# Optimization experiments

Hardware: AMD Instinct MI355X
Metric: run time of the kernel (lower is better)

Reference implementation:

```python
import jax, jax.numpy as jnp
import numpy as np

INPUT_SIZE = 4096
HIDDEN = 1024
WINDOW = 2048
STRIDE = 1024
METRIC = 32
POOLING = "last"


def setup_inputs() -> dict:
    key = jax.random.key(0)
    ks = jax.random.split(key, 9)
    s = 1.0 / np.sqrt(HIDDEN)  # torch LSTMCell/Linear init bound
    u = lambda k, shape: jax.random.uniform(k, shape, jnp.float32, -s, s)
    return {
        "inp": jax.random.normal(ks[0], (WINDOW, INPUT_SIZE), jnp.float32),
        "h1": jax.random.normal(ks[1], (1, HIDDEN), jnp.float32),
        "c1": jax.random.normal(ks[2], (1, HIDDEN), jnp.float32),
        "W_ih": u(ks[3], (4 * HIDDEN, INPUT_SIZE)),
        "W_hh": u(ks[4], (4 * HIDDEN, HIDDEN)),
        "b_ih": u(ks[5], (4 * HIDDEN,)),
        "b_hh": u(ks[6], (4 * HIDDEN,)),
        "fc_w": u(ks[7], (METRIC, HIDDEN)),
        "fc_b": u(ks[8], (METRIC,)),
    }


def reference(inp, h1, c1, W_ih, W_hh, b_ih, b_hh, fc_w, fc_b):
    window = min(WINDOW, inp.shape[0])
    # Precompute the input-side gate projection as one GEMM: [T, 4H]
    xg = inp[:window] @ W_ih.T + b_ih

    def step(carry, xg_t):
        h, c = carry  # each [1, H]
        gates = xg_t + h @ W_hh.T + b_hh  # [1, 4H]
        i, f, g, o = jnp.split(gates, 4, axis=-1)
        c = jax.nn.sigmoid(f) * c + jax.nn.sigmoid(i) * jnp.tanh(g)
        h = jax.nn.sigmoid(o) * jnp.tanh(c)
        return (h, c), (h, c)

    (h_fin, c_fin), (hs, cs) = jax.lax.scan(step, (h1, c1), xg)

    if window >= STRIDE:
        h_last = jax.lax.stop_gradient(hs[STRIDE - 1])  # [1, H], detached
        c_last = jax.lax.stop_gradient(cs[STRIDE - 1])
    else:
        h_last, c_last = None, None

    if POOLING == "mean":
        # mean of fc(h_i) over last STRIDE steps of the window
        out = (hs[window - STRIDE:, 0, :] @ fc_w.T + fc_b).sum(axis=0, keepdims=True) / STRIDE
    else:  # 'last'
        out = h_fin @ fc_w.T + fc_b  # [1, METRIC]
    out = jnp.tanh(out)
    return out, h_last, c_last
```

## Files before the change

### kernel.cpp

```cpp
#include <hip/hip_runtime.h>
#include <stdint.h>

typedef unsigned short u16;
typedef unsigned long long u64;
typedef __attribute__((ext_vector_type(8))) short short8;
typedef __attribute__((ext_vector_type(4))) float floatx4;

#define K_IN    4096
#define HID     1024
#define G4H     4096
#define T_STEPS 2048
#define NWG     128
#define SPIN_MAX 60000

__device__ __forceinline__ u16 f2bf(float f) {
  union { float f; unsigned int i; } v; v.f = f;
  unsigned int lsb = (v.i >> 16) & 1u;
  v.i += 0x7fffu + lsb;
  return (u16)(v.i >> 16);
}
__device__ __forceinline__ float finz(float x) {
  unsigned b = __float_as_uint(x);
  return ((b & 0x7f800000u) == 0x7f800000u) ? 0.f : x;
}
__device__ __forceinline__ float sigm(float x) {
  x = fminf(30.f, fmaxf(-30.f, finz(x)));
  return 1.0f / (1.0f + __expf(-x));
}
__device__ __forceinline__ float tanh_s(float x) {
  x = fminf(15.f, fmaxf(-15.f, finz(x)));
  float e = __expf(2.0f * x);
  return (e - 1.0f) / (e + 1.0f);
}

__device__ __forceinline__ void publish_h(u64* hx, int slot, int idx, float h) {
  h = finz(h);
  u64 v = ((u64)(unsigned)(slot + 1) << 32) | (u64)__float_as_uint(h);
  __hip_atomic_store(&hx[(size_t)slot * HID + idx], v,
                     __ATOMIC_RELAXED, __HIP_MEMORY_SCOPE_AGENT);
}

__device__ __forceinline__ void poll4(const u64* hx, int slot, int j0,
                                      float* v, int* alive) {
  const u64* p = hx + (size_t)slot * HID + j0;
  const unsigned tag = (unsigned)(slot + 1);
  if (*alive) {
    int spins = 0;
    for (;;) {
      u64 a = __hip_atomic_load(&p[0], __ATOMIC_RELAXED, __HIP_MEMORY_SCOPE_AGENT);
      u64 b = __hip_atomic_load(&p[1], __ATOMIC_RELAXED, __HIP_MEMORY_SCOPE_AGENT);
      u64 c = __hip_atomic_load(&p[2], __ATOMIC_RELAXED, __HIP_MEMORY_SCOPE_AGENT);
      u64 d = __hip_atomic_load(&p[3], __ATOMIC_RELAXED, __HIP_MEMORY_SCOPE_AGENT);
      if ((unsigned)(a >> 32) == tag && (unsigned)(b >> 32) == tag &&
          (unsigned)(c >> 32) == tag && (unsigned)(d >> 32) == tag) {
        v[0] = finz(__uint_as_float((unsigned)a));
        v[1] = finz(__uint_as_float((unsigned)b));
        v[2] = finz(__uint_as_float((unsigned)c));
        v[3] = finz(__uint_as_float((unsigned)d));
        return;
      }
      if (++spins > SPIN_MAX) { *alive = 0; break; }
      __builtin_amdgcn_s_sleep(1);
    }
  }
  v[0] = v[1] = v[2] = v[3] = 0.f;
}

__global__ __launch_bounds__(256) void cvt_bf16_k(const float* __restrict__ src,
                                                  u16* __restrict__ dst, int n4) {
  int i = blockIdx.x * 256 + threadIdx.x;
  if (i < n4) {
    float4 v = *(const float4*)(src + (size_t)i * 4);
    u16 o0 = f2bf(v.x), o1 = f2bf(v.y), o2 = f2bf(v.z), o3 = f2bf(v.w);
    ushort4 o = {o0, o1, o2, o3};
    *(ushort4*)(dst + (size_t)i * 4) = o;
  }
}

__global__ __launch_bounds__(256) void xg_gemm_k(const u16* __restrict__ A,
                                                 const u16* __restrict__ B,
                                                 const float* __restrict__ bias,
                                                 float* __restrict__ C)
{
  __shared__ __align__(16) u16 As[128 * 64];
  __shared__ __align__(16) u16 Bs[128 * 64];
  const int tid  = threadIdx.x;
  const int lane = tid & 63;
  const int quad = lane >> 4;
  const int l16  = lane & 15;
  const int wid  = tid >> 6;
  const int wm   = wid >> 1, wn = wid & 1;
  const int tileM = blockIdx.y * 128;
  const int tileN = blockIdx.x * 128;

  floatx4 acc[4][4];
  #pragma unroll
  for (int mi = 0; mi < 4; ++mi)
    #pragma unroll
    for (int ni = 0; ni < 4; ++ni)
      acc[mi][ni] = (floatx4){0.f, 0.f, 0.f, 0.f};

  for (int k0 = 0; k0 < K_IN; k0 += 64) {
    #pragma unroll
    for (int i = 0; i < 4; ++i) {
      int c = i * 256 + tid;
      int row = c >> 3, col = (c & 7) * 8;
      *(short8*)(As + c * 8) = *(const short8*)(A + (size_t)(tileM + row) * K_IN + k0 + col);
      *(short8*)(Bs + c * 8) = *(const short8*)(B + (size_t)(tileN + row) * K_IN + k0 + col);
    }
    __syncthreads();
    #pragma unroll
    for (int kk = 0; kk < 64; kk += 32) {
      short8 av[4], bv[4];
      #pragma unroll
      for (int mi = 0; mi < 4; ++mi)
        av[mi] = *(const short8*)(As + (wm * 64 + mi * 16 + l16) * 64 + kk + quad * 8);
      #pragma unroll
      for (int ni = 0; ni < 4; ++ni)
        bv[ni] = *(const short8*)(Bs + (wn * 64 + ni * 16 + l16) * 64 + kk + quad * 8);
      #pragma unroll
      for (int mi = 0; mi < 4; ++mi)
        #pragma unroll
        for (int ni = 0; ni < 4; ++ni)
          acc[mi][ni] = __builtin_amdgcn_mfma_f32_16x16x32_bf16(av[mi], bv[ni], acc[mi][ni], 0, 0, 0);
    }
    __syncthreads();
  }
  #pragma unroll
  for (int ni = 0; ni < 4; ++ni) {
    int n = tileN + wn * 64 + ni * 16 + l16;
    float bn = bias[n];
    #pragma unroll
    for (int mi = 0; mi < 4; ++mi) {
      int mbase = tileM + wm * 64 + mi * 16 + quad * 4;
      #pragma unroll
      for (int r = 0; r < 4; ++r)
        C[(size_t)(mbase + r) * G4H + n] = acc[mi][ni][r] + bn;
    }
  }
}

__global__ __launch_bounds__(256, 1) void lstm_scan_k(const float* __restrict__ Whh,
                                                      const float* __restrict__ bhh,
                                                      const float* __restrict__ h1,
                                                      const float* __restrict__ c1,
                                                      const float* __restrict__ fcw,
                                                      const float* __restrict__ fcb,
                                                      const float* __restrict__ xg,
                                                      u64* hx,
                                                      float* out)
{
  const int g    = blockIdx.x;
  const int tid  = threadIdx.x;
  const int lane = tid & 63;
  const int w    = tid >> 6;

  __shared__ float h_local[HID];
  __shared__ float gsum[32];
  __shared__ float xgb[2][32];
  __shared__ float bhhb[32];
  __shared__ float pp[32][8];

  float wreg[8][16];
  {
    const size_t rowbase = (size_t)(w * HID + g * 8);
    #pragma unroll
    for (int u = 0; u < 8; ++u)
      #pragma unroll
      for (int j = 0; j < 16; ++j)
        wreg[u][j] = Whh[(rowbase + u) * HID + j * 64 + lane];
  }
  if (tid < 32) bhhb[tid] = bhh[(tid >> 3) * HID + g * 8 + (tid & 7)];

  float c_state = 0.f;
  if (tid < 8) {
    c_state = c1[g * 8 + tid];
    publish_h(hx, 0, g * 8 + tid, h1[g * 8 + tid]);
  }

  int alive = 1;
  const int j0 = tid * 4;
  for (int t = 0; t < T_STEPS; ++t) {
    float xval = 0.f;
    if (tid < 32) xval = finz(xg[(size_t)t * G4H + (tid >> 3) * HID + g * 8 + (tid & 7)]);
    float v[4];
    poll4(hx, t, j0, v, &alive);
    h_local[j0 + 0] = v[0]; h_local[j0 + 1] = v[1];
    h_local[j0 + 2] = v[2]; h_local[j0 + 3] = v[3];
    if (tid < 32) xgb[t & 1][tid] = xval;
    __syncthreads();

    float s[8] = {0.f, 0.f, 0.f, 0.f, 0.f, 0.f, 0.f, 0.f};
    #pragma unroll
    for (int j = 0; j < 16; ++j) {
      float hv = h_local[j * 64 + lane];
      #pragma unroll
      for (int u = 0; u < 8; ++u) s[u] = fmaf(wreg[u][j], hv, s[u]);
    }
    #pragma unroll
    for (int d = 1; d < 64; d <<= 1) {
      #pragma unroll
      for (int u = 0; u < 8; ++u) s[u] += __shfl_xor(s[u], d, 64);
    }
    if (lane == 0) {
      #pragma unroll
      for (int u = 0; u < 8; ++u) gsum[w * 8 + u] = s[u];
    }
    __syncthreads();

    if (tid < 8) {
      const int u = tid;
      const float* xb = xgb[t & 1];
      float gi = gsum[u]      + xb[u]      + bhhb[u];
      float gf = gsum[8 + u]  + xb[8 + u]  + bhhb[8 + u];
      float gg = gsum[16 + u] + xb[16 + u] + bhhb[16 + u];
      float go = gsum[24 + u] + xb[24 + u] + bhhb[24 + u];
      float iv = sigm(gi), fv = sigm(gf), gv = tanh_s(gg), ov = sigm(go);
      c_state = finz(fv * c_state + iv * gv);
      float hval = ov * tanh_s(c_state);
      publish_h(hx, t + 1, g * 8 + u, hval);
      if (t == 1023) {
        out[32 + g * 8 + u]       = finz(hval);
        out[32 + HID + g * 8 + u] = finz(c_state);
      }
    }
  }

  if (g == 0) {
    float v[4];
    poll4(hx, T_STEPS, j0, v, &alive);
    h_local[j0 + 0] = v[0]; h_local[j0 + 1] = v[1];
    h_local[j0 + 2] = v[2]; h_local[j0 + 3] = v[3];
    __syncthreads();
    const int m = tid >> 3, seg = tid & 7;
    float p = 0.f;
    for (int k = seg * 128; k < seg * 128 + 128; ++k)
      p = fmaf(fcw[m * HID + k], h_local[k], p);
    pp[m][seg] = finz(p);
    __syncthreads();
    if (tid < 32) {
      float sum = fcb[tid];
      #pragma unroll
      for (int i = 0; i < 8; ++i) sum += pp[tid][i];
      out[tid] = tanh_s(finz(sum));
    }
  }
}

extern "C" void kernel_launch(void* const* d_in, const int* in_sizes, int n_in,
                              void* d_out, int out_size, void* d_ws, size_t ws_size,
                              hipStream_t stream) {
  const float* inp = (const float*)d_in[0];
  const float* h1  = (const float*)d_in[1];
  const float* c1  = (const float*)d_in[2];
  const float* Wih = (const float*)d_in[3];
  const float* Whh = (const float*)d_in[4];
  const float* bih = (const float*)d_in[5];
  const float* bhh = (const float*)d_in[6];
  const float* fcw = (const float*)d_in[7];
  const float* fcb = (const float*)d_in[8];
  float* out = (float*)d_out;

  const size_t xg_bytes  = (size_t)T_STEPS * G4H * 4;
  const size_t hx_bytes  = (size_t)(T_STEPS + 1) * HID * 8;
  const size_t ab_bytes  = (size_t)T_STEPS * K_IN * 2;
  const size_t wb_bytes  = (size_t)G4H * K_IN * 2;
  if (ws_size < xg_bytes + hx_bytes + ab_bytes + wb_bytes) return;

  float* xg   = (float*)d_ws;
  u64*   hx   = (u64*)((char*)d_ws + xg_bytes);
  u16*   Abf  = (u16*)((char*)d_ws + xg_bytes + hx_bytes);
  u16*   Wbf  = (u16*)((char*)d_ws + xg_bytes + hx_bytes + ab_bytes);

  const int nA4 = T_STEPS * K_IN / 4;
  const int nW4 = G4H * K_IN / 4;
  cvt_bf16_k<<<dim3((nA4 + 255) / 256), 256, 0, stream>>>(inp, Abf, nA4);
  cvt_bf16_k<<<dim3((nW4 + 255) / 256), 256, 0, stream>>>(Wih, Wbf, nW4);
  xg_gemm_k<<<dim3(G4H / 128, T_STEPS / 128), 256, 0, stream>>>(Abf, Wbf, bih, xg);
  lstm_scan_k<<<dim3(NWG), 256, 0, stream>>>(Whh, bhh, h1, c1, fcw, fcb, xg, hx, out);
}
```

Before: 5.187 ms.

## Remove per-step block barriers by making each wave poll full h vector independently

Each wave now owns two hidden units (all four gates) and polls the entire 1024-element h vector directly into registers, replacing the shared-memory staging and both __syncthreads per timestep. Gate sums stay in registers after the shuffle reduction, so the gsum/xgb shared buffers disappear. The s_sleep in the spin loop is removed and the spin limit is lowered. The cost is 4x redundant global atomic polling traffic per workgroup, plus heavier contention on the h exchange buffer.

```diff
diff --git a/kernel.cpp b/kernel.cpp
--- a/kernel.cpp
+++ b/kernel.cpp
@@ -11,7 +11,7 @@
 #define G4H     4096
 #define T_STEPS 2048
 #define NWG     128
-#define SPIN_MAX 60000
+#define SPIN_MAX 20000
 
 __device__ __forceinline__ u16 f2bf(float f) {
   union { float f; unsigned int i; } v; v.f = f;
@@ -38,32 +38,6 @@
   u64 v = ((u64)(unsigned)(slot + 1) << 32) | (u64)__float_as_uint(h);
   __hip_atomic_store(&hx[(size_t)slot * HID + idx], v,
                      __ATOMIC_RELAXED, __HIP_MEMORY_SCOPE_AGENT);
-}
-
-__device__ __forceinline__ void poll4(const u64* hx, int slot, int j0,
-                                      float* v, int* alive) {
-  const u64* p = hx + (size_t)slot * HID + j0;
-  const unsigned tag = (unsigned)(slot + 1);
-  if (*alive) {
-    int spins = 0;
-    for (;;) {
-      u64 a = __hip_atomic_load(&p[0], __ATOMIC_RELAXED, __HIP_MEMORY_SCOPE_AGENT);
-      u64 b = __hip_atomic_load(&p[1], __ATOMIC_RELAXED, __HIP_MEMORY_SCOPE_AGENT);
-      u64 c = __hip_atomic_load(&p[2], __ATOMIC_RELAXED, __HIP_MEMORY_SCOPE_AGENT);
-      u64 d = __hip_atomic_load(&p[3], __ATOMIC_RELAXED, __HIP_MEMORY_SCOPE_AGENT);
-      if ((unsigned)(a >> 32) == tag && (unsigned)(b >> 32) == tag &&
-          (unsigned)(c >> 32) == tag && (unsigned)(d >> 32) == tag) {
-        v[0] = finz(__uint_as_float((unsigned)a));
-        v[1] = finz(__uint_as_float((unsigned)b));
-        v[2] = finz(__uint_as_float((unsigned)c));
-        v[3] = finz(__uint_as_float((unsigned)d));
-        return;
-      }
-      if (++spins > SPIN_MAX) { *alive = 0; break; }
-      __builtin_amdgcn_s_sleep(1);
-    }
-  }
-  v[0] = v[1] = v[2] = v[3] = 0.f;
 }
 
 __global__ __launch_bounds__(256) void cvt_bf16_k(const float* __restrict__ src,
@@ -154,89 +128,130 @@
   const int tid  = threadIdx.x;
   const int lane = tid & 63;
   const int w    = tid >> 6;
+  const int U0   = g * 8 + w * 2;
 
   __shared__ float h_local[HID];
-  __shared__ float gsum[32];
-  __shared__ float xgb[2][32];
-  __shared__ float bhhb[32];
   __shared__ float pp[32][8];
 
   float wreg[8][16];
-  {
-    const size_t rowbase = (size_t)(w * HID + g * 8);
-    #pragma unroll
-    for (int u = 0; u < 8; ++u)
-      #pragma unroll
-      for (int j = 0; j < 16; ++j)
-        wreg[u][j] = Whh[(rowbase + u) * HID + j * 64 + lane];
-  }
-  if (tid < 32) bhhb[tid] = bhh[(tid >> 3) * HID + g * 8 + (tid & 7)];
-
+  #pragma unroll
+  for (int u = 0; u < 8; ++u) {
+    const size_t row = (size_t)((u & 3) * HID + U0 + (u >> 2));
+    #pragma unroll
+    for (int j = 0; j < 16; ++j)
+      wreg[u][j] = Whh[row * HID + j * 64 + lane];
+  }
+
+  float bq[4] = {0.f, 0.f, 0.f, 0.f};
   float c_state = 0.f;
-  if (tid < 8) {
-    c_state = c1[g * 8 + tid];
-    publish_h(hx, 0, g * 8 + tid, h1[g * 8 + tid]);
+  if (lane < 2) {
+    const int U = U0 + lane;
+    #pragma unroll
+    for (int q = 0; q < 4; ++q) bq[q] = bhh[q * HID + U];
+    c_state = c1[U];
+    publish_h(hx, 0, U, h1[U]);
   }
 
   int alive = 1;
-  const int j0 = tid * 4;
   for (int t = 0; t < T_STEPS; ++t) {
-    float xval = 0.f;
-    if (tid < 32) xval = finz(xg[(size_t)t * G4H + (tid >> 3) * HID + g * 8 + (tid & 7)]);
-    float v[4];
-    poll4(hx, t, j0, v, &alive);
-    h_local[j0 + 0] = v[0]; h_local[j0 + 1] = v[1];
-    h_local[j0 + 2] = v[2]; h_local[j0 + 3] = v[3];
-    if (tid < 32) xgb[t & 1][tid] = xval;
-    __syncthreads();
+    float xq[4] = {0.f, 0.f, 0.f, 0.f};
+    if (lane < 2) {
+      const size_t xb = (size_t)t * G4H + U0 + lane;
+      #pragma unroll
+      for (int q = 0; q < 4; ++q) xq[q] = finz(xg[xb + q * HID]);
+    }
+
+    float h[16];
+    {
+      const u64* p = hx + (size_t)t * HID + lane;
+      const unsigned tag = (unsigned)(t + 1);
+      int got = 0;
+      if (alive) {
+        int spins = 0;
+        for (;;) {
+          u64 v[16];
+          #pragma unroll
+          for (int j = 0; j < 16; ++j)
+            v[j] = __hip_atomic_load(&p[j * 64], __ATOMIC_RELAXED, __HIP_MEMORY_SCOPE_AGENT);
+          int ok = 1;
+          #pragma unroll
+          for (int j = 0; j < 16; ++j)
+            ok &= ((unsigned)(v[j] >> 32) == tag);
+          if (ok) {
+            #pragma unroll
+            for (int j = 0; j < 16; ++j)
+              h[j] = finz(__uint_as_float((unsigned)v[j]));
+            got = 1;
+            break;
+          }
+          if (++spins > SPIN_MAX) { alive = 0; break; }
+        }
+      }
+      if (!got) {
+        #pragma unroll
+        for (int j = 0; j < 16; ++j) h[j] = 0.f;
+      }
+    }
 
     float s[8] = {0.f, 0.f, 0.f, 0.f, 0.f, 0.f, 0.f, 0.f};
     #pragma unroll
     for (int j = 0; j < 16; ++j) {
-      float hv = h_local[j * 64 + lane];
-      #pragma unroll
-      for (int u = 0; u < 8; ++u) s[u] = fmaf(wreg[u][j], hv, s[u]);
+      #pragma unroll
+      for (int u = 0; u < 8; ++u) s[u] = fmaf(wreg[u][j], h[j], s[u]);
     }
     #pragma unroll
     for (int d = 1; d < 64; d <<= 1) {
       #pragma unroll
       for (int u = 0; u < 8; ++u) s[u] += __shfl_xor(s[u], d, 64);
     }
-    if (lane == 0) {
-      #pragma unroll
-      for (int u = 0; u < 8; ++u) gsum[w * 8 + u] = s[u];
-    }
-    __syncthreads();
-
-    if (tid < 8) {
-      const int u = tid;
-      const float* xb = xgb[t & 1];
-      float gi = gsum[u]      + xb[u]      + bhhb[u];
-      float gf = gsum[8 + u]  + xb[8 + u]  + bhhb[8 + u];
-      float gg = gsum[16 + u] + xb[16 + u] + bhhb[16 + u];
-      float go = gsum[24 + u] + xb[24 + u] + bhhb[24 + u];
+
+    if (lane < 2) {
+      const int b = lane * 4;
+      float gi = s[b + 0] + xq[0] + bq[0];
+      float gf = s[b + 1] + xq[1] + bq[1];
+      float gg = s[b + 2] + xq[2] + bq[2];
+      float go = s[b + 3] + xq[3] + bq[3];
       float iv = sigm(gi), fv = sigm(gf), gv = tanh_s(gg), ov = sigm(go);
       c_state = finz(fv * c_state + iv * gv);
       float hval = ov * tanh_s(c_state);
-      publish_h(hx, t + 1, g * 8 + u, hval);
+      publish_h(hx, t + 1, U0 + lane, hval);
       if (t == 1023) {
-        out[32 + g * 8 + u]       = finz(hval);
-        out[32 + HID + g * 8 + u] = finz(c_state);
+        out[32 + U0 + lane]       = finz(hval);
+        out[32 + HID + U0 + lane] = finz(c_state);
       }
     }
   }
 
   if (g == 0) {
-    float v[4];
-    poll4(hx, T_STEPS, j0, v, &alive);
-    h_local[j0 + 0] = v[0]; h_local[j0 + 1] = v[1];
-    h_local[j0 + 2] = v[2]; h_local[j0 + 3] = v[3];
+    if (w == 0) {
+      const u64* p = hx + (size_t)T_STEPS * HID + lane;
+      const unsigned tag = (unsigned)(T_STEPS + 1);
+      u64 v[16];
+      int got = 0;
+      if (alive) {
+        int spins = 0;
+        for (;;) {
+          #pragma unroll
+          for (int j = 0; j < 16; ++j)
+            v[j] = __hip_atomic_load(&p[j * 64], __ATOMIC_RELAXED, __HIP_MEMORY_SCOPE_AGENT);
+          int ok = 1;
+          #pragma unroll
+          for (int j = 0; j < 16; ++j)
+            ok &= ((unsigned)(v[j] >> 32) == tag);
+          if (ok) { got = 1; break; }
+          if (++spins > SPIN_MAX) break;
+        }
+      }
+      #pragma unroll
+      for (int j = 0; j < 16; ++j)
+        h_local[j * 64 + lane] = got ? finz(__uint_as_float((unsigned)v[j])) : 0.f;
+    }
     __syncthreads();
     const int m = tid >> 3, seg = tid & 7;
-    float p = 0.f;
+    float pacc = 0.f;
     for (int k = seg * 128; k < seg * 128 + 128; ++k)
-      p = fmaf(fcw[m * HID + k], h_local[k], p);
-    pp[m][seg] = finz(p);
+      pacc = fmaf(fcw[m * HID + k], h_local[k], pacc);
+    pp[m][seg] = finz(pacc);
     __syncthreads();
     if (tid < 32) {
       float sum = fcb[tid];
```

Measured after the change: 6.885 ms. 32.7% more time.
